# Optimization experiments

Measured on AMD Instinct MI355X. Metric: run time of the kernel, lower is better.

Reference implementation:

```python
import jax, jax.numpy as jnp
import numpy as np

B, S, D_IN = 2, 2048, 2048
H, G, D = 16, 4, 128  # heads, kv groups, head_dim
EPS = 1e-6


def rms_norm(x, w):
    # RMSNorm over last dim (head_dim), computed in fp32
    xf = x.astype(jnp.float32)
    var = jnp.mean(xf * xf, axis=-1, keepdims=True)
    return (xf * jax.lax.rsqrt(var + EPS) * w).astype(x.dtype)


def apply_rope(x, cos, sin):
    # x: [b, h, s, d]; cos/sin: [s, d]
    half = x.shape[-1] // 2
    x1, x2 = x[..., :half], x[..., half:]
    rotated = jnp.concatenate([-x2, x1], axis=-1)
    return x * cos[None, None] + rotated * sin[None, None]


def setup_inputs() -> dict:
    key = jax.random.key(0)
    ks = jax.random.split(key, 8)
    x = jax.random.normal(ks[0], (B, S, D_IN), jnp.float32)
    # causal mask: True above the diagonal (masked positions)
    mask = jnp.triu(jnp.ones((S, S), dtype=bool), k=1)
    # RoPE tables: duplicated half-dim frequencies
    inv_freq = 1.0 / (10000.0 ** (np.arange(0, D, 2, dtype=np.float32) / D))
    angles = np.arange(S, dtype=np.float32)[:, None] * inv_freq[None, :]  # [S, D/2]
    angles = np.concatenate([angles, angles], axis=-1)  # [S, D]
    cos = jnp.asarray(np.cos(angles))
    sin = jnp.asarray(np.sin(angles))
    sc = 0.02
    Wq = jax.random.normal(ks[1], (D_IN, H * D), jnp.float32) * sc
    Wk = jax.random.normal(ks[2], (D_IN, G * D), jnp.float32) * sc
    Wv = jax.random.normal(ks[3], (D_IN, G * D), jnp.float32) * sc
    Wo = jax.random.normal(ks[4], (H * D, D_IN), jnp.float32) * sc
    q_norm_w = jnp.ones((D,), jnp.float32)
    k_norm_w = jnp.ones((D,), jnp.float32)
    return {"x": x, "mask": mask, "cos": cos, "sin": sin, "Wq": Wq, "Wk": Wk,
            "Wv": Wv, "Wo": Wo, "q_norm_w": q_norm_w, "k_norm_w": k_norm_w}


def reference(x, mask, cos, sin, Wq, Wk, Wv, Wo, q_norm_w, k_norm_w):
    b, s, _ = x.shape
    scaling = D ** -0.5
    q = (x @ Wq).reshape(b, s, H, D).transpose(0, 2, 1, 3)  # [b,H,s,D]
    k = (x @ Wk).reshape(b, s, G, D).transpose(0, 2, 1, 3)  # [b,G,s,D]
    v = (x @ Wv).reshape(b, s, G, D).transpose(0, 2, 1, 3)
    q = rms_norm(q, q_norm_w)
    k = rms_norm(k, k_norm_w)
    q = apply_rope(q, cos, sin)
    k = apply_rope(k, cos, sin)
    # GQA: repeat_interleave KV groups to full head count
    k = jnp.repeat(k, H // G, axis=1)  # [b,H,s,D]
    v = jnp.repeat(v, H // G, axis=1)
    scores = jnp.einsum('bhqd,bhkd->bhqk', q * scaling, k)
    scores = jnp.where(mask[None, None], -jnp.inf, scores)
    attn = jax.nn.softmax(scores.astype(jnp.float32), axis=-1).astype(q.dtype)
    ctx = jnp.einsum('bhqk,bhkd->bhqd', attn, v)
    ctx = ctx.transpose(0, 2, 1, 3).reshape(b, s, H * D)
    return ctx @ Wo
```

## Files before the change

### kernel.cpp

```cpp
#include <hip/hip_runtime.h>
#include <stdint.h>


typedef __attribute__((ext_vector_type(8))) short short8;
typedef __attribute__((ext_vector_type(4))) float f32x4;

__device__ __forceinline__ unsigned short f2bf(float f) {
  unsigned int u = __builtin_bit_cast(unsigned int, f);
  u += 0x7fffu + ((u >> 16) & 1u);
  return (unsigned short)(u >> 16);
}

__device__ __forceinline__ void gl_lds16(const void* g, void* l) {
  __builtin_amdgcn_global_load_lds(
      (const __attribute__((address_space(1))) unsigned int*)g,
      (__attribute__((address_space(3))) unsigned int*)l, 16, 0, 0);
}

__global__ __launch_bounds__(256) void k_cast_x(const float* __restrict__ x,
                                                unsigned short* __restrict__ xb) {
  int t = blockIdx.x * 256 + threadIdx.x;
  int m = t >> 8;
  int c = t & 255;
  const float* src = x + ((size_t)m * 2048 + (size_t)c * 8);
  float4 a = *(const float4*)src;
  float4 b = *(const float4*)(src + 4);
  uint4 o;
  o.x = f2bf(a.x) | ((unsigned)f2bf(a.y) << 16);
  o.y = f2bf(a.z) | ((unsigned)f2bf(a.w) << 16);
  o.z = f2bf(b.x) | ((unsigned)f2bf(b.y) << 16);
  o.w = f2bf(b.z) | ((unsigned)f2bf(b.w) << 16);
  *(uint4*)(xb + (size_t)m * 2048 + (size_t)((c ^ (m & 7)) * 8)) = o;
}

__global__ __launch_bounds__(256) void k_wtrans(const float* __restrict__ W,
                                                unsigned short* __restrict__ WT,
                                                int K, int N) {
  __shared__ float tile[64][65];
  int k0 = blockIdx.x * 64, n0 = blockIdx.y * 64;
  int c = threadIdx.x & 63, r0 = threadIdx.x >> 6;
#pragma unroll
  for (int i = 0; i < 16; i++) {
    int kl = r0 + i * 4;
    tile[kl][c] = W[(size_t)(k0 + kl) * N + n0 + c];
  }
  __syncthreads();
#pragma unroll
  for (int i = 0; i < 16; i++) {
    int nl = r0 + i * 4;
    int n = n0 + nl;
    int sw = (n & 7) << 3;
    WT[(size_t)n * K + (size_t)((k0 + c) ^ sw)] = f2bf(tile[c][nl]);
  }
}

__global__ __launch_bounds__(256) void k_vtrans(const float* __restrict__ qkv,
                                                unsigned short* __restrict__ vts) {
  __shared__ float tile[64][65];
  int bg = blockIdx.z;
  int s0 = blockIdx.x * 64, d0 = blockIdx.y * 64;
  int b = bg >> 2, g = bg & 3;
  int c = threadIdx.x & 63, r0 = threadIdx.x >> 6;
#pragma unroll
  for (int i = 0; i < 16; i++) {
    int sl = r0 + i * 4;
    tile[sl][c] = qkv[(size_t)(b * 2048 + s0 + sl) * 3072 + 2560 + g * 128 + d0 + c];
  }
  __syncthreads();
#pragma unroll
  for (int i = 0; i < 16; i++) {
    int dl = r0 + i * 4;
    int d = d0 + dl;
    int sw = (d & 7) << 3;
    vts[((size_t)(bg * 128 + d)) * 2048 + (size_t)((s0 + c) ^ sw)] = f2bf(tile[c][dl]);
  }
}

__global__ __launch_bounds__(256) void k_norm_rope(const float* __restrict__ qkv,
                                                   const float* __restrict__ cosT,
                                                   const float* __restrict__ sinT,
                                                   const float* __restrict__ qw,
                                                   const float* __restrict__ kw,
                                                   unsigned short* __restrict__ qh,
                                                   unsigned short* __restrict__ khs) {
  int wid = blockIdx.x * 4 + (threadIdx.x >> 6);
  int lane = threadIdx.x & 63;
  int slot = wid % 20;
  int token = wid / 20;
  int b = token >> 11, s = token & 2047;
  int colbase = (slot < 16) ? slot * 128 : 2048 + (slot - 16) * 128;
  const float* base = qkv + (size_t)token * 3072 + colbase;
  float x1 = base[lane], x2 = base[lane + 64];
  float ss = x1 * x1 + x2 * x2;
#pragma unroll
  for (int o = 1; o < 64; o <<= 1) ss += __shfl_xor(ss, o);
  float rr = rsqrtf(ss * (1.0f / 128.0f) + 1e-6f);
  const float* wv = (slot < 16) ? qw : kw;
  float y1 = x1 * rr * wv[lane];
  float y2 = x2 * rr * wv[lane + 64];
  float c1 = cosT[s * 128 + lane], s1 = sinT[s * 128 + lane];
  float c2 = cosT[s * 128 + lane + 64], s2 = sinT[s * 128 + lane + 64];
  float o1 = y1 * c1 - y2 * s1;
  float o2 = y2 * c2 + y1 * s2;
  if (slot < 16) {
    const float sc = 0.08838834764831845f;
    unsigned short* dst = qh + ((size_t)((b * 16 + slot) * 2048 + s)) * 128;
    dst[lane] = f2bf(o1 * sc);
    dst[lane + 64] = f2bf(o2 * sc);
  } else {
    int g = slot - 16;
    unsigned short* dst = khs + ((size_t)((b * 4 + g) * 2048 + s)) * 128;
    int sw = (s & 7) << 3;
    dst[lane ^ sw] = f2bf(o1);
    dst[(lane + 64) ^ sw] = f2bf(o2);
  }
}

__global__ __launch_bounds__(256, 2) void k_gemm(const unsigned short* __restrict__ A,
                                                 const unsigned short* __restrict__ Bt,
                                                 float* __restrict__ C,
                                                 int M, int N, int K, int tilesN) {
  __shared__ unsigned short lA[2][128 * 64];
  __shared__ unsigned short lB[2][128 * 64];
  int nwg = gridDim.x;
  int cpx = nwg >> 3;
  int bid = blockIdx.x;
  int wg = (bid & 7) * cpx + (bid >> 3);
  int tm = wg / tilesN, tn = wg - tm * tilesN;
  int m0 = tm << 7, n0 = tn << 7;
  int tid = threadIdx.x;
  int w = tid >> 6, l = tid & 63;
  int lo = l & 15, hi = l >> 4;
  int srow = tid >> 3, schunk = (tid & 7) * 8;
  int wr = (w >> 1) * 64, wc = (w & 1) * 64;
  int xorv = (l & 7) << 3;
  int nt = K >> 6;
  f32x4 acc[4][4];
#pragma unroll
  for (int i = 0; i < 4; i++)
#pragma unroll
    for (int j = 0; j < 4; j++) acc[i][j] = (f32x4){0.f, 0.f, 0.f, 0.f};

  auto stage = [&](int buf, int t) {
    int k0 = t << 6;
#pragma unroll
    for (int i = 0; i < 4; i++) {
      gl_lds16(A + (size_t)(m0 + i * 32 + srow) * (size_t)K + k0 + schunk,
               &lA[buf][(i * 32 + w * 8) * 64]);
      gl_lds16(Bt + (size_t)(n0 + i * 32 + srow) * (size_t)K + k0 + schunk,
               &lB[buf][(i * 32 + w * 8) * 64]);
    }
  };

  stage(0, 0);
  __syncthreads();
  int cur = 0;
  for (int t = 0; t < nt; t++) {
    if (t + 1 < nt) stage(cur ^ 1, t + 1);
#pragma unroll
    for (int kk = 0; kk < 2; kk++) {
      short8 af[4], bfv[4];
#pragma unroll
      for (int i = 0; i < 4; i++) {
        af[i] = *(const short8*)&lA[cur][(wr + i * 16 + lo) * 64 + ((kk * 32 + hi * 8) ^ xorv)];
        bfv[i] = *(const short8*)&lB[cur][(wc + i * 16 + lo) * 64 + ((kk * 32 + hi * 8) ^ xorv)];
      }
#pragma unroll
      for (int i = 0; i < 4; i++)
#pragma unroll
        for (int j = 0; j < 4; j++)
          acc[i][j] = __builtin_amdgcn_mfma_f32_16x16x32_bf16(af[i], bfv[j], acc[i][j], 0, 0, 0);
    }
    __syncthreads();
    cur ^= 1;
  }
#pragma unroll
  for (int i = 0; i < 4; i++)
#pragma unroll
    for (int j = 0; j < 4; j++)
#pragma unroll
      for (int r = 0; r < 4; r++)
        C[(size_t)(m0 + wr + i * 16 + hi * 4 + r) * (size_t)N + (n0 + wc + j * 16 + lo)] =
            acc[i][j][r];
}

__global__ __launch_bounds__(256, 2) void k_attn(const unsigned short* __restrict__ qh,
                                                 const unsigned short* __restrict__ khs,
                                                 const unsigned short* __restrict__ vts,
                                                 unsigned short* __restrict__ ctx) {
  __shared__ unsigned short p_lds[4][32 * 64];

  int bid = blockIdx.x;
  int b = bid >> 8;
  int h = (bid >> 4) & 15;
  int qt = bid & 15;
  int g = h >> 2;
  int tid = threadIdx.x, w = tid >> 6, l = tid & 63;
  int lo = l & 15, hi = l >> 4, xorv = (l & 7) << 3;
  int q0 = qt * 128 + w * 32;

  const unsigned short* kg = khs + ((size_t)(b * 4 + g)) * 2048 * 128;
  const unsigned short* vg = vts + ((size_t)(b * 4 + g)) * 128 * 2048;

  short8 qf[2][4];
#pragma unroll
  for (int mi = 0; mi < 2; mi++)
#pragma unroll
    for (int kd = 0; kd < 4; kd++)
      qf[mi][kd] = *(const short8*)(qh +
          ((size_t)((b * 16 + h) * 2048 + q0 + mi * 16 + lo)) * 128 + kd * 32 + hi * 8);

  f32x4 accO[2][8];
#pragma unroll
  for (int mi = 0; mi < 2; mi++)
#pragma unroll
    for (int nj = 0; nj < 8; nj++) accO[mi][nj] = (f32x4){0.f, 0.f, 0.f, 0.f};
  float lrun[2][4];
#pragma unroll
  for (int mi = 0; mi < 2; mi++)
#pragma unroll
    for (int r = 0; r < 4; r++) lrun[mi][r] = 0.f;

  int nt = ((q0 + 31) >> 6) + 1;
  for (int t = 0; t < nt; t++) {
    int s0 = t << 6;

    short8 bf[4][4];
#pragma unroll
    for (int ni = 0; ni < 4; ni++) {
      int row = ni * 16 + lo;
      int sw = (row & 7) << 3;
#pragma unroll
      for (int kd = 0; kd < 4; kd++)
        bf[kd][ni] = *(const short8*)(kg + (size_t)(s0 + row) * 128 + ((kd * 32 + hi * 8) ^ sw));
    }

    f32x4 sc[2][4];
#pragma unroll
    for (int mi = 0; mi < 2; mi++)
#pragma unroll
      for (int ni = 0; ni < 4; ni++) sc[mi][ni] = (f32x4){0.f, 0.f, 0.f, 0.f};
#pragma unroll
    for (int kd = 0; kd < 4; kd++)
#pragma unroll
      for (int ni = 0; ni < 4; ni++) {
        sc[0][ni] = __builtin_amdgcn_mfma_f32_16x16x32_bf16(qf[0][kd], bf[kd][ni], sc[0][ni], 0, 0, 0);
        sc[1][ni] = __builtin_amdgcn_mfma_f32_16x16x32_bf16(qf[1][kd], bf[kd][ni], sc[1][ni], 0, 0, 0);
      }

    short8 bv[2][8];
#pragma unroll
    for (int nj = 0; nj < 8; nj++) {
      int d = nj * 16 + lo;
      int swv = (d & 7) << 3;
#pragma unroll
      for (int kt = 0; kt < 2; kt++)
        bv[kt][nj] = *(const short8*)(vg + (size_t)d * 2048 + ((s0 + kt * 32 + hi * 8) ^ swv));
    }

    if (t == nt - 1) {
#pragma unroll
      for (int mi = 0; mi < 2; mi++)
#pragma unroll
        for (int ni = 0; ni < 4; ni++)
#pragma unroll
          for (int r = 0; r < 4; r++) {
            int qrow = q0 + mi * 16 + hi * 4 + r;
            int col = s0 + ni * 16 + lo;
            if (col > qrow) sc[mi][ni][r] = -1e30f;
          }
    }

#pragma unroll
    for (int mi = 0; mi < 2; mi++)
#pragma unroll
      for (int ni = 0; ni < 4; ni++)
#pragma unroll
        for (int r = 0; r < 4; r++) {
          float p = __expf(sc[mi][ni][r]);
          lrun[mi][r] += p;
          int rp = mi * 16 + hi * 4 + r;
          int cp = ni * 16 + lo;
          p_lds[w][rp * 64 + (cp ^ ((rp & 7) << 3))] = f2bf(p);
        }

#pragma unroll
    for (int kt = 0; kt < 2; kt++) {
      short8 pa0 = *(const short8*)&p_lds[w][(lo) * 64 + ((kt * 32 + hi * 8) ^ xorv)];
      short8 pa1 = *(const short8*)&p_lds[w][(16 + lo) * 64 + ((kt * 32 + hi * 8) ^ xorv)];
#pragma unroll
      for (int nj = 0; nj < 8; nj++) {
        accO[0][nj] = __builtin_amdgcn_mfma_f32_16x16x32_bf16(pa0, bv[kt][nj], accO[0][nj], 0, 0, 0);
        accO[1][nj] = __builtin_amdgcn_mfma_f32_16x16x32_bf16(pa1, bv[kt][nj], accO[1][nj], 0, 0, 0);
      }
    }
  }

#pragma unroll
  for (int mi = 0; mi < 2; mi++)
#pragma unroll
    for (int r = 0; r < 4; r++) {
      float s = lrun[mi][r];
      s += __shfl_xor(s, 1);
      s += __shfl_xor(s, 2);
      s += __shfl_xor(s, 4);
      s += __shfl_xor(s, 8);
      lrun[mi][r] = s;
    }

#pragma unroll
  for (int mi = 0; mi < 2; mi++)
#pragma unroll
    for (int r = 0; r < 4; r++) {
      float inv = 1.0f / lrun[mi][r];
      int row = b * 2048 + q0 + mi * 16 + hi * 4 + r;
      int sw = (row & 7) << 3;
#pragma unroll
      for (int nj = 0; nj < 8; nj++) {
        int col = h * 128 + nj * 16 + lo;
        ctx[(size_t)row * 2048 + (size_t)(col ^ sw)] = f2bf(accO[mi][nj][r] * inv);
      }
    }
}

extern "C" void kernel_launch(void* const* d_in, const int* in_sizes, int n_in,
                              void* d_out, int out_size, void* d_ws, size_t ws_size,
                              hipStream_t stream) {
  const float* x    = (const float*)d_in[0];
  const float* cosT = (const float*)d_in[2];
  const float* sinT = (const float*)d_in[3];
  const float* Wq   = (const float*)d_in[4];
  const float* Wk   = (const float*)d_in[5];
  const float* Wv   = (const float*)d_in[6];
  const float* Wo   = (const float*)d_in[7];
  const float* qw   = (const float*)d_in[8];
  const float* kw   = (const float*)d_in[9];
  float* out = (float*)d_out;

  char* ws = (char*)d_ws;
  unsigned short* xb    = (unsigned short*)ws; ws += (size_t)4096 * 2048 * 2;
  unsigned short* wqkvT = (unsigned short*)ws; ws += (size_t)3072 * 2048 * 2;
  unsigned short* woT   = (unsigned short*)ws; ws += (size_t)2048 * 2048 * 2;
  float*          qkv   = (float*)ws;          ws += (size_t)4096 * 3072 * 4;
  unsigned short* qh    = (unsigned short*)ws; ws += (size_t)2 * 16 * 2048 * 128 * 2;
  unsigned short* khs   = (unsigned short*)ws; ws += (size_t)2 * 4 * 2048 * 128 * 2;
  unsigned short* vts   = (unsigned short*)ws; ws += (size_t)2 * 4 * 2048 * 128 * 2;
  unsigned short* ctx   = (unsigned short*)ws; ws += (size_t)4096 * 2048 * 2;

  k_cast_x<<<4096, 256, 0, stream>>>(x, xb);
  k_wtrans<<<dim3(32, 32), 256, 0, stream>>>(Wq, wqkvT, 2048, 2048);
  k_wtrans<<<dim3(32, 8),  256, 0, stream>>>(Wk, wqkvT + (size_t)2048 * 2048, 2048, 512);
  k_wtrans<<<dim3(32, 8),  256, 0, stream>>>(Wv, wqkvT + (size_t)2560 * 2048, 2048, 512);
  k_wtrans<<<dim3(32, 32), 256, 0, stream>>>(Wo, woT, 2048, 2048);

  k_gemm<<<768, 256, 0, stream>>>(xb, wqkvT, qkv, 4096, 3072, 2048, 24);
  k_norm_rope<<<20480, 256, 0, stream>>>(qkv, cosT, sinT, qw, kw, qh, khs);
  k_vtrans<<<dim3(32, 2, 8), 256, 0, stream>>>(qkv, vts);
  k_attn<<<512, 256, 0, stream>>>(qh, khs, vts, ctx);
  k_gemm<<<512, 256, 0, stream>>>(ctx, woT, out, 4096, 2048, 2048, 16);
}
```

Before: 444.7 us.

## Split long causal attention rows across two blocks and combine partial results

Reorganizes the attention grid so each block handles one KV group with its four heads per warp, sharing K/V tiles, and processes query tiles longest-first. Query tiles in the second half of the sequence have their KV range split in two, written as unnormalized fp32 partials plus row sums, and merged by a new combine kernel. This targets load imbalance from causal masking and the tail of the grid, at the cost of extra partial-result memory traffic, an extra launch, and reuse of the qkv buffer as scratch.

New measurement: 401.2 us. 1.11x faster.

```diff
diff --git a/kernel.cpp b/kernel.cpp
--- a/kernel.cpp
+++ b/kernel.cpp
@@ -187,17 +187,36 @@
 __global__ __launch_bounds__(256, 2) void k_attn(const unsigned short* __restrict__ qh,
                                                  const unsigned short* __restrict__ khs,
                                                  const unsigned short* __restrict__ vts,
-                                                 unsigned short* __restrict__ ctx) {
+                                                 unsigned short* __restrict__ ctx,
+                                                 float* __restrict__ Opart,
+                                                 float* __restrict__ lsumPart) {
   __shared__ unsigned short p_lds[4][32 * 64];
 
   int bid = blockIdx.x;
-  int b = bid >> 8;
-  int h = (bid >> 4) & 15;
-  int qt = bid & 15;
-  int g = h >> 2;
+  int bg = bid & 7, j = bid >> 3;
+  int b = bg >> 2, g = bg & 3;
   int tid = threadIdx.x, w = tid >> 6, l = tid & 63;
+  int h = g * 4 + w;
   int lo = l & 15, hi = l >> 4, xorv = (l & 7) << 3;
-  int q0 = qt * 128 + w * 32;
+
+  int qt32, t0, t1;
+  bool partial;
+  int slot = j & 1;
+  if (j < 64) {
+    qt32 = 63 - (j >> 1);
+    int nt = (qt32 >> 1) + 1;
+    int half = nt >> 1;
+    t0 = slot ? half : 0;
+    t1 = slot ? nt : half;
+    partial = true;
+  } else {
+    qt32 = 95 - j;
+    t0 = 0;
+    t1 = (qt32 >> 1) + 1;
+    partial = false;
+  }
+  int q0 = qt32 * 32;
+  int ntm1 = qt32 >> 1;
 
   const unsigned short* kg = khs + ((size_t)(b * 4 + g)) * 2048 * 128;
   const unsigned short* vg = vts + ((size_t)(b * 4 + g)) * 128 * 2048;
@@ -221,8 +240,7 @@
 #pragma unroll
     for (int r = 0; r < 4; r++) lrun[mi][r] = 0.f;
 
-  int nt = ((q0 + 31) >> 6) + 1;
-  for (int t = 0; t < nt; t++) {
+  for (int t = t0; t < t1; t++) {
     int s0 = t << 6;
 
     short8 bf[4][4];
@@ -258,7 +276,7 @@
         bv[kt][nj] = *(const short8*)(vg + (size_t)d * 2048 + ((s0 + kt * 32 + hi * 8) ^ swv));
     }
 
-    if (t == nt - 1) {
+    if (t == ntm1) {
 #pragma unroll
       for (int mi = 0; mi < 2; mi++)
 #pragma unroll
@@ -308,19 +326,60 @@
       lrun[mi][r] = s;
     }
 
-#pragma unroll
-  for (int mi = 0; mi < 2; mi++)
-#pragma unroll
-    for (int r = 0; r < 4; r++) {
-      float inv = 1.0f / lrun[mi][r];
-      int row = b * 2048 + q0 + mi * 16 + hi * 4 + r;
-      int sw = (row & 7) << 3;
-#pragma unroll
-      for (int nj = 0; nj < 8; nj++) {
-        int col = h * 128 + nj * 16 + lo;
-        ctx[(size_t)row * 2048 + (size_t)(col ^ sw)] = f2bf(accO[mi][nj][r] * inv);
+  if (!partial) {
+#pragma unroll
+    for (int mi = 0; mi < 2; mi++)
+#pragma unroll
+      for (int r = 0; r < 4; r++) {
+        float inv = 1.0f / lrun[mi][r];
+        int row = b * 2048 + q0 + mi * 16 + hi * 4 + r;
+        int sw = (row & 7) << 3;
+#pragma unroll
+        for (int nj = 0; nj < 8; nj++) {
+          int col = h * 128 + nj * 16 + lo;
+          ctx[(size_t)row * 2048 + (size_t)(col ^ sw)] = f2bf(accO[mi][nj][r] * inv);
+        }
       }
-    }
+  } else {
+    float* Ob = Opart + ((((size_t)slot * 2 + b) * 16 + h) * 1024) * 128;
+#pragma unroll
+    for (int mi = 0; mi < 2; mi++)
+#pragma unroll
+      for (int r = 0; r < 4; r++) {
+        int srel = q0 - 1024 + mi * 16 + hi * 4 + r;
+#pragma unroll
+        for (int nj = 0; nj < 8; nj++)
+          Ob[(size_t)srel * 128 + nj * 16 + lo] = accO[mi][nj][r];
+        if (lo == 0)
+          lsumPart[(((size_t)slot * 2 + b) * 16 + h) * 1024 + srel] = lrun[mi][r];
+      }
+  }
+}
+
+__global__ __launch_bounds__(256) void k_combine(const float* __restrict__ Opart,
+                                                 const float* __restrict__ lsumPart,
+                                                 unsigned short* __restrict__ ctx) {
+  const size_t SLOT = (size_t)2 * 16 * 1024 * 128;
+  int t = blockIdx.x * 256 + threadIdx.x;
+  int d4 = t & 31;
+  int srel = (t >> 5) & 1023;
+  int h = (t >> 15) & 15;
+  int b = (t >> 19) & 1;
+  size_t base = (((size_t)b * 16 + h) * 1024 + srel) * 128 + d4 * 4;
+  float4 o0 = *(const float4*)(Opart + base);
+  float4 o1 = *(const float4*)(Opart + SLOT + base);
+  size_t lidx = ((size_t)b * 16 + h) * 1024 + srel;
+  float inv = 1.0f / (lsumPart[lidx] + lsumPart[(size_t)2 * 16 * 1024 + lidx]);
+  int s = 1024 + srel;
+  int row = b * 2048 + s;
+  int col = h * 128 + d4 * 4;
+  int sw = (s & 7) << 3;
+  ushort4 o;
+  o.x = f2bf((o0.x + o1.x) * inv);
+  o.y = f2bf((o0.y + o1.y) * inv);
+  o.z = f2bf((o0.z + o1.z) * inv);
+  o.w = f2bf((o0.w + o1.w) * inv);
+  *(ushort4*)(ctx + (size_t)row * 2048 + (size_t)(col ^ sw)) = o;
 }
 
 extern "C" void kernel_launch(void* const* d_in, const int* in_sizes, int n_in,
@@ -346,6 +405,8 @@
   unsigned short* khs   = (unsigned short*)ws; ws += (size_t)2 * 4 * 2048 * 128 * 2;
   unsigned short* vts   = (unsigned short*)ws; ws += (size_t)2 * 4 * 2048 * 128 * 2;
   unsigned short* ctx   = (unsigned short*)ws; ws += (size_t)4096 * 2048 * 2;
+  float*       lsumPart = (float*)ws;          ws += (size_t)2 * 2 * 16 * 1024 * 4;
+  float* Opart = qkv;
 
   k_cast_x<<<4096, 256, 0, stream>>>(x, xb);
   k_wtrans<<<dim3(32, 32), 256, 0, stream>>>(Wq, wqkvT, 2048, 2048);
@@ -356,6 +417,7 @@
   k_gemm<<<768, 256, 0, stream>>>(xb, wqkvT, qkv, 4096, 3072, 2048, 24);
   k_norm_rope<<<20480, 256, 0, stream>>>(qkv, cosT, sinT, qw, kw, qh, khs);
   k_vtrans<<<dim3(32, 2, 8), 256, 0, stream>>>(qkv, vts);
-  k_attn<<<512, 256, 0, stream>>>(qh, khs, vts, ctx);
+  k_attn<<<768, 256, 0, stream>>>(qh, khs, vts, ctx, Opart, lsumPart);
+  k_combine<<<4096, 256, 0, stream>>>(Opart, lsumPart, ctx);
   k_gemm<<<512, 256, 0, stream>>>(ctx, woT, out, 4096, 2048, 2048, 16);
 }
```
